# Kernel optimization log

Measured on AMD Instinct MI355X. Metric: run time of the kernel, lower is better.

The kernel has to match this reference:

```python
import jax, jax.numpy as jnp
import numpy as np

B, D = 8192, 1024

def setup_inputs() -> dict:
    key = jax.random.key(0)
    ks = jax.random.split(key, 5)
    scale = 1.0 / np.sqrt(D)
    return {
        "x": jax.random.normal(ks[0], (B, D), dtype=jnp.float32),
        "h": jax.random.normal(ks[1], (B, D), dtype=jnp.float32),
        "c": jax.random.normal(ks[2], (B, D), dtype=jnp.float32),
        # gate order: [input, forget, output, candidate]
        "Wx": jax.random.normal(ks[3], (4, D, D), dtype=jnp.float32) * scale,
        "Wh": jax.random.normal(ks[4], (4, D, D), dtype=jnp.float32) * scale,
    }

def reference(x, h, c, Wx, Wh):
    # two batched GEMMs covering all 8 projections: [B,D] x [4,D,D] -> [4,B,D]
    gx = jnp.einsum('bd,gdk->gbk', x, Wx)
    gh = jnp.einsum('bd,gdk->gbk', h, Wh)
    g = gx + gh
    i = jax.nn.sigmoid(g[0])
    f = jax.nn.sigmoid(g[1])
    o = jax.nn.sigmoid(g[2])
    u = jnp.tanh(g[3])
    c_t = i * u + f * c
    h_t = o * jnp.tanh(c_t)
    return (h_t, c_t)
```

## Files before the change

kernel.cpp:

```cpp
#include <hip/hip_runtime.h>
#include <hip/hip_bf16.h>
#include <cstdint>


#define LDS_TOTAL 131072

typedef __attribute__((ext_vector_type(8))) short bf16x8;
typedef __attribute__((ext_vector_type(4))) float f32x4;
typedef __attribute__((ext_vector_type(4))) unsigned int u32x4;

static __device__ __forceinline__ unsigned short f2bf(float f) {
  union { float f; unsigned int u; } v; v.f = f;
  unsigned int u = v.u;
  unsigned int r = (u + 0x7FFFu + ((u >> 16) & 1u)) >> 16;
  return (unsigned short)r;
}

static __device__ __forceinline__ void load16(const void* gp, void* lp) {
  __builtin_amdgcn_global_load_lds(
      (const __attribute__((address_space(1))) void*)gp,
      (__attribute__((address_space(3))) void*)lp, 16, 0, 0);
}

static __device__ __forceinline__ float sigmoid_f(float x) {
  return 1.0f / (1.0f + __expf(-x));
}
static __device__ __forceinline__ float tanh_f(float x) {
  float e = __expf(-2.0f * fabsf(x));
  float r = (1.0f - e) / (1.0f + e);
  return copysignf(r, x);
}

__global__ __launch_bounds__(256) void pack_a_kernel(
    const float* __restrict__ x, const float* __restrict__ h,
    unsigned short* __restrict__ Apack) {
  int t = blockIdx.x * 256 + threadIdx.x;
  size_t base = (size_t)t * 8;
  int b = (int)(base >> 11);
  int k = (int)(base & 2047);
  const float* src = (k < 1024) ? (x + (size_t)b * 1024 + k)
                                : (h + (size_t)b * 1024 + (k - 1024));
  float4 v0 = ((const float4*)src)[0];
  float4 v1 = ((const float4*)src)[1];
  union { unsigned short s[8]; u32x4 v; } o;
  o.s[0] = f2bf(v0.x); o.s[1] = f2bf(v0.y); o.s[2] = f2bf(v0.z); o.s[3] = f2bf(v0.w);
  o.s[4] = f2bf(v1.x); o.s[5] = f2bf(v1.y); o.s[6] = f2bf(v1.z); o.s[7] = f2bf(v1.w);
  *(u32x4*)(Apack + base) = o.v;
}

__global__ __launch_bounds__(256) void prep_w_kernel(
    const float* __restrict__ Wx, const float* __restrict__ Wh,
    unsigned short* __restrict__ Wt) {
  __shared__ float tile[32][33];
  int bid = blockIdx.x;
  int g = bid >> 11;
  int rem = bid & 2047;
  int kt = rem >> 5;
  int nt = rem & 31;
  int k0 = kt * 32, n0 = nt * 32;
  int tx = threadIdx.x & 31, ty = threadIdx.x >> 5;
  const float* Wsrc;
  int ks;
  if (k0 < 1024) { Wsrc = Wx + (size_t)g * 1048576; ks = k0; }
  else           { Wsrc = Wh + (size_t)g * 1048576; ks = k0 - 1024; }
  #pragma unroll
  for (int s = 0; s < 4; ++s) {
    int r = ty + s * 8;
    tile[r][tx] = Wsrc[(size_t)(ks + r) * 1024 + n0 + tx];
  }
  __syncthreads();
  #pragma unroll
  for (int s = 0; s < 4; ++s) {
    int r = ty + s * 8;
    Wt[(size_t)((g << 10) + n0 + r) * 2048 + k0 + tx] = f2bf(tile[tx][r]);
  }
}

__global__ __launch_bounds__(512, 2) void lstm_gemm_kernel(
    const unsigned short* __restrict__ Apack,
    const unsigned short* __restrict__ Wt,
    const float* __restrict__ cprev,
    float* __restrict__ out) {
  extern __shared__ char lds[];
  const int tid = threadIdx.x;
  const int l = tid & 63;
  const int w = tid >> 6;
  const int wr = w >> 2;
  const int wc = w & 3;
  const int bid0 = blockIdx.x;
  const int bid = (bid0 & 7) * 64 + (bid0 >> 3);
  const int mt = bid >> 4;
  const int nt = bid & 15;
  const int m0 = mt << 8;
  const int n0 = nt << 6;

  char* const buf0 = lds;
  char* const buf1 = lds + 65536;

  f32x4 acc[8][4];
  #pragma unroll
  for (int mf = 0; mf < 8; ++mf)
    #pragma unroll
    for (int g = 0; g < 4; ++g) acc[mf][g] = (f32x4)0.0f;

  bf16x8 aR[4][2];
  bf16x8 bR[4][2];

  const int lr = l & 15;
  const int kgrp = (l >> 4) << 4;
  const int sx = (lr & 7) << 4;
  const int kx0 = kgrp ^ sx;
  const int kx1 = (64 + kgrp) ^ sx;
  const int aoff = (wr * 128 + lr) * 128;
  const int boff = 32768 + (wc * 16 + lr) * 128;

  const int arl = tid >> 3;
  const int akb = ((tid << 4) & 127) ^ ((arl & 7) << 4);
  const unsigned short* const gAbase =
      Apack + (size_t)(m0 + arl) * 2048 + (akb >> 1);
  const int dAbase = (tid & ~63) << 4;
  const unsigned short* const gBbase =
      Wt + (size_t)(n0 + arl) * 2048 + (akb >> 1);
  const int dBbase = 32768 + ((tid & ~63) << 4);

  auto stageA = [&](char* bufb, int h, int kstep) {
    const unsigned short* g0 = gAbase + ((size_t)h * 262144 + (kstep << 6));
    #pragma unroll
    for (int j = 0; j < 2; ++j)
      load16(g0 + (size_t)j * 131072,
             bufb + dAbase + h * 16384 + j * 8192);
  };
  auto stageB = [&](char* bufb, int h, int kstep) {
    const unsigned short* g0 = gBbase + ((size_t)(2 * h) * 2097152 + (kstep << 6));
    #pragma unroll
    for (int j = 0; j < 2; ++j)
      load16(g0 + (size_t)j * 2097152,
             bufb + dBbase + h * 16384 + j * 8192);
  };

  auto readA = [&](const char* bufc, int mh) {
    #pragma unroll
    for (int i = 0; i < 4; ++i) {
      const char* p = bufc + aoff + (mh * 64 + i * 16) * 128;
      aR[i][0] = *(const bf16x8*)(p + kx0);
      aR[i][1] = *(const bf16x8*)(p + kx1);
    }
  };
  auto readB = [&](const char* bufc, int gh) {
    #pragma unroll
    for (int i = 0; i < 2; ++i) {
      const char* p = bufc + boff + (gh * 2 + i) * 8192;
      bR[gh * 2 + i][0] = *(const bf16x8*)(p + kx0);
      bR[gh * 2 + i][1] = *(const bf16x8*)(p + kx1);
    }
  };
  auto mfma16 = [&](int mh, int gh) {
    __builtin_amdgcn_s_setprio(1);
    #pragma unroll
    for (int kk = 0; kk < 2; ++kk)
      #pragma unroll
      for (int i = 0; i < 4; ++i)
        #pragma unroll
        for (int gg = 0; gg < 2; ++gg)
          acc[mh * 4 + i][gh * 2 + gg] = __builtin_amdgcn_mfma_f32_16x16x32_bf16(
              aR[i][kk], bR[gh * 2 + gg][kk], acc[mh * 4 + i][gh * 2 + gg], 0, 0, 0);
    __builtin_amdgcn_s_setprio(0);
  };

  stageA(buf0, 0, 0); stageA(buf0, 1, 0);
  stageB(buf0, 0, 0); stageB(buf0, 1, 0);
  stageB(buf1, 0, 1); stageB(buf1, 1, 1);
  stageA(buf1, 0, 1);
  asm volatile("s_waitcnt vmcnt(6)" ::: "memory");
  __builtin_amdgcn_s_barrier();

  auto kstep = [&](int t, char* bufc, char* bufn) {
    readA(bufc, 0);
    readB(bufc, 0);
    if (t + 1 < 32) stageA(bufn, 1, t + 1);
    asm volatile("s_waitcnt lgkmcnt(8)" ::: "memory");
    __builtin_amdgcn_s_barrier();
    asm volatile("s_waitcnt lgkmcnt(0)" ::: "memory");
    mfma16(0, 0);
    __builtin_amdgcn_s_barrier();
    readB(bufc, 1);
    if (t + 2 < 32) stageB(bufc, 0, t + 2);
    __builtin_amdgcn_s_barrier();
    asm volatile("s_waitcnt lgkmcnt(0)" ::: "memory");
    mfma16(0, 1);
    __builtin_amdgcn_s_barrier();
    readA(bufc, 1);
    if (t + 2 < 32) stageB(bufc, 1, t + 2);
    __builtin_amdgcn_s_barrier();
    asm volatile("s_waitcnt lgkmcnt(0)" ::: "memory");
    mfma16(1, 1);
    __builtin_amdgcn_s_barrier();
    if (t + 2 < 32) stageA(bufc, 0, t + 2);
    if (t < 30) asm volatile("s_waitcnt vmcnt(6)" ::: "memory");
    else        asm volatile("s_waitcnt vmcnt(0)" ::: "memory");
    __builtin_amdgcn_s_barrier();
    mfma16(1, 0);
    __builtin_amdgcn_s_barrier();
  };

  #pragma unroll 1
  for (int tt = 0; tt < 16; ++tt) {
    kstep(2 * tt,     buf0, buf1);
    kstep(2 * tt + 1, buf1, buf0);
  }

  const int q = (l >> 4) << 2;
  const int col = n0 + wc * 16 + lr;
  #pragma unroll
  for (int mf = 0; mf < 8; ++mf) {
    #pragma unroll
    for (int j = 0; j < 4; ++j) {
      int row = m0 + wr * 128 + mf * 16 + q + j;
      float gi = acc[mf][0][j];
      float gf = acc[mf][1][j];
      float go = acc[mf][2][j];
      float gu = acc[mf][3][j];
      float i_ = sigmoid_f(gi);
      float f_ = sigmoid_f(gf);
      float o_ = sigmoid_f(go);
      float u_ = tanh_f(gu);
      size_t idx = (size_t)row * 1024 + col;
      float ct = i_ * u_ + f_ * cprev[idx];
      float ht = o_ * tanh_f(ct);
      out[idx] = ht;
      out[8388608 + idx] = ct;
    }
  }
}

extern "C" void kernel_launch(void* const* d_in, const int* in_sizes, int n_in,
                              void* d_out, int out_size, void* d_ws, size_t ws_size,
                              hipStream_t stream) {
  const float* x  = (const float*)d_in[0];
  const float* h  = (const float*)d_in[1];
  const float* c  = (const float*)d_in[2];
  const float* Wx = (const float*)d_in[3];
  const float* Wh = (const float*)d_in[4];
  float* out = (float*)d_out;

  unsigned short* Apack = (unsigned short*)d_ws;
  unsigned short* Wt = (unsigned short*)((char*)d_ws + 33554432);

  hipFuncSetAttribute((const void*)lstm_gemm_kernel,
                      hipFuncAttributeMaxDynamicSharedMemorySize, LDS_TOTAL);

  pack_a_kernel<<<8192, 256, 0, stream>>>(x, h, Apack);
  prep_w_kernel<<<8192, 256, 0, stream>>>(Wx, Wh, Wt);
  lstm_gemm_kernel<<<dim3(512), dim3(512), LDS_TOTAL, stream>>>(Apack, Wt, c, out);
}
```

Baseline: 158.7 us.

## Shrink GEMM block tile to 128x32 with 256 threads and 2048 blocks

Halves the workgroup tile in both M and N (256x64x4 gates to 128x32x4 gates), uses 4 waves per block instead of 8, and launches 2048 blocks with 64KB of LDS instead of 512 blocks with 128KB. The k-step pipeline is restructured into two MFMA phases with new staging offsets. The aim is more blocks resident per CU and better load balance across CUs. The cost is lower arithmetic intensity per block, so each block reloads more A and W data from global memory for the same work.

After: 185.0 us. 16.6% more time.

```diff
diff --git a/kernel.cpp b/kernel.cpp
--- a/kernel.cpp
+++ b/kernel.cpp
@@ -3,7 +3,7 @@
 #include <cstdint>
 
 
-#define LDS_TOTAL 131072
+#define LDS_TOTAL 65536
 
 typedef __attribute__((ext_vector_type(8))) short bf16x8;
 typedef __attribute__((ext_vector_type(4))) float f32x4;
@@ -76,7 +76,7 @@
   }
 }
 
-__global__ __launch_bounds__(512, 2) void lstm_gemm_kernel(
+__global__ __launch_bounds__(256, 2) void lstm_gemm_kernel(
     const unsigned short* __restrict__ Apack,
     const unsigned short* __restrict__ Wt,
     const float* __restrict__ cprev,
@@ -85,21 +85,21 @@
   const int tid = threadIdx.x;
   const int l = tid & 63;
   const int w = tid >> 6;
-  const int wr = w >> 2;
-  const int wc = w & 3;
+  const int wr = w >> 1;
+  const int wc = w & 1;
   const int bid0 = blockIdx.x;
-  const int bid = (bid0 & 7) * 64 + (bid0 >> 3);
-  const int mt = bid >> 4;
-  const int nt = bid & 15;
-  const int m0 = mt << 8;
-  const int n0 = nt << 6;
+  const int bid = (bid0 & 7) * 256 + (bid0 >> 3);
+  const int mt = bid >> 5;
+  const int nt = bid & 31;
+  const int m0 = mt << 7;
+  const int n0 = nt << 5;
 
   char* const buf0 = lds;
-  char* const buf1 = lds + 65536;
-
-  f32x4 acc[8][4];
-  #pragma unroll
-  for (int mf = 0; mf < 8; ++mf)
+  char* const buf1 = lds + 32768;
+
+  f32x4 acc[4][4];
+  #pragma unroll
+  for (int mf = 0; mf < 4; ++mf)
     #pragma unroll
     for (int g = 0; g < 4; ++g) acc[mf][g] = (f32x4)0.0f;
 
@@ -111,37 +111,39 @@
   const int sx = (lr & 7) << 4;
   const int kx0 = kgrp ^ sx;
   const int kx1 = (64 + kgrp) ^ sx;
-  const int aoff = (wr * 128 + lr) * 128;
-  const int boff = 32768 + (wc * 16 + lr) * 128;
+  const int aoff = (wr * 64 + lr) * 128;
+  const int boff = 16384 + (wc * 16 + lr) * 128;
 
   const int arl = tid >> 3;
   const int akb = ((tid << 4) & 127) ^ ((arl & 7) << 4);
   const unsigned short* const gAbase =
       Apack + (size_t)(m0 + arl) * 2048 + (akb >> 1);
-  const int dAbase = (tid & ~63) << 4;
   const unsigned short* const gBbase =
       Wt + (size_t)(n0 + arl) * 2048 + (akb >> 1);
-  const int dBbase = 32768 + ((tid & ~63) << 4);
-
-  auto stageA = [&](char* bufb, int h, int kstep) {
-    const unsigned short* g0 = gAbase + ((size_t)h * 262144 + (kstep << 6));
-    #pragma unroll
-    for (int j = 0; j < 2; ++j)
-      load16(g0 + (size_t)j * 131072,
-             bufb + dAbase + h * 16384 + j * 8192);
-  };
-  auto stageB = [&](char* bufb, int h, int kstep) {
-    const unsigned short* g0 = gBbase + ((size_t)(2 * h) * 2097152 + (kstep << 6));
-    #pragma unroll
-    for (int j = 0; j < 2; ++j)
-      load16(g0 + (size_t)j * 2097152,
-             bufb + dBbase + h * 16384 + j * 8192);
-  };
-
-  auto readA = [&](const char* bufc, int mh) {
+  const int dbase = (tid & ~63) << 4;
+
+  auto stageA = [&](char* bufb, int t) {
+    const unsigned short* g0 = gAbase + (t << 6);
+    load16(g0,          bufb + dbase);
+    load16(g0 +  65536, bufb + dbase + 4096);
+    load16(g0 + 131072, bufb + dbase + 8192);
+    load16(g0 + 196608, bufb + dbase + 12288);
+  };
+  auto stageB0 = [&](char* bufb, int t) {
+    const unsigned short* g0 = gBbase + (t << 6);
+    load16(g0,           bufb + 16384 + dbase);
+    load16(g0 + 2097152, bufb + 20480 + dbase);
+  };
+  auto stageB1 = [&](char* bufb, int t) {
+    const unsigned short* g0 = gBbase + (size_t)2 * 2097152 + (t << 6);
+    load16(g0,           bufb + 24576 + dbase);
+    load16(g0 + 2097152, bufb + 28672 + dbase);
+  };
+
+  auto readA = [&](const char* bufc) {
     #pragma unroll
     for (int i = 0; i < 4; ++i) {
-      const char* p = bufc + aoff + (mh * 64 + i * 16) * 128;
+      const char* p = bufc + aoff + i * 2048;
       aR[i][0] = *(const bf16x8*)(p + kx0);
       aR[i][1] = *(const bf16x8*)(p + kx1);
     }
@@ -149,12 +151,12 @@
   auto readB = [&](const char* bufc, int gh) {
     #pragma unroll
     for (int i = 0; i < 2; ++i) {
-      const char* p = bufc + boff + (gh * 2 + i) * 8192;
+      const char* p = bufc + boff + (gh * 2 + i) * 4096;
       bR[gh * 2 + i][0] = *(const bf16x8*)(p + kx0);
       bR[gh * 2 + i][1] = *(const bf16x8*)(p + kx1);
     }
   };
-  auto mfma16 = [&](int mh, int gh) {
+  auto mfma16 = [&](int gh) {
     __builtin_amdgcn_s_setprio(1);
     #pragma unroll
     for (int kk = 0; kk < 2; ++kk)
@@ -162,44 +164,32 @@
       for (int i = 0; i < 4; ++i)
         #pragma unroll
         for (int gg = 0; gg < 2; ++gg)
-          acc[mh * 4 + i][gh * 2 + gg] = __builtin_amdgcn_mfma_f32_16x16x32_bf16(
-              aR[i][kk], bR[gh * 2 + gg][kk], acc[mh * 4 + i][gh * 2 + gg], 0, 0, 0);
+          acc[i][gh * 2 + gg] = __builtin_amdgcn_mfma_f32_16x16x32_bf16(
+              aR[i][kk], bR[gh * 2 + gg][kk], acc[i][gh * 2 + gg], 0, 0, 0);
     __builtin_amdgcn_s_setprio(0);
   };
 
-  stageA(buf0, 0, 0); stageA(buf0, 1, 0);
-  stageB(buf0, 0, 0); stageB(buf0, 1, 0);
-  stageB(buf1, 0, 1); stageB(buf1, 1, 1);
-  stageA(buf1, 0, 1);
+  stageA(buf0, 0); stageB0(buf0, 0); stageB1(buf0, 0);
+  stageA(buf1, 1); stageB0(buf1, 1);
   asm volatile("s_waitcnt vmcnt(6)" ::: "memory");
   __builtin_amdgcn_s_barrier();
 
   auto kstep = [&](int t, char* bufc, char* bufn) {
-    readA(bufc, 0);
+    readA(bufc);
     readB(bufc, 0);
-    if (t + 1 < 32) stageA(bufn, 1, t + 1);
+    if (t + 1 < 32) stageB1(bufn, t + 1);
     asm volatile("s_waitcnt lgkmcnt(8)" ::: "memory");
     __builtin_amdgcn_s_barrier();
     asm volatile("s_waitcnt lgkmcnt(0)" ::: "memory");
-    mfma16(0, 0);
+    mfma16(0);
     __builtin_amdgcn_s_barrier();
     readB(bufc, 1);
-    if (t + 2 < 32) stageB(bufc, 0, t + 2);
+    if (t + 2 < 32) { stageA(bufc, t + 2); stageB0(bufc, t + 2); }
     __builtin_amdgcn_s_barrier();
     asm volatile("s_waitcnt lgkmcnt(0)" ::: "memory");
-    mfma16(0, 1);
-    __builtin_amdgcn_s_barrier();
-    readA(bufc, 1);
-    if (t + 2 < 32) stageB(bufc, 1, t + 2);
-    __builtin_amdgcn_s_barrier();
-    asm volatile("s_waitcnt lgkmcnt(0)" ::: "memory");
-    mfma16(1, 1);
-    __builtin_amdgcn_s_barrier();
-    if (t + 2 < 32) stageA(bufc, 0, t + 2);
+    mfma16(1);
     if (t < 30) asm volatile("s_waitcnt vmcnt(6)" ::: "memory");
     else        asm volatile("s_waitcnt vmcnt(0)" ::: "memory");
-    __builtin_amdgcn_s_barrier();
-    mfma16(1, 0);
     __builtin_amdgcn_s_barrier();
   };
 
@@ -212,10 +202,10 @@
   const int q = (l >> 4) << 2;
   const int col = n0 + wc * 16 + lr;
   #pragma unroll
-  for (int mf = 0; mf < 8; ++mf) {
+  for (int mf = 0; mf < 4; ++mf) {
     #pragma unroll
     for (int j = 0; j < 4; ++j) {
-      int row = m0 + wr * 128 + mf * 16 + q + j;
+      int row = m0 + wr * 64 + mf * 16 + q + j;
       float gi = acc[mf][0][j];
       float gf = acc[mf][1][j];
       float go = acc[mf][2][j];
@@ -246,10 +236,7 @@
   unsigned short* Apack = (unsigned short*)d_ws;
   unsigned short* Wt = (unsigned short*)((char*)d_ws + 33554432);
 
-  hipFuncSetAttribute((const void*)lstm_gemm_kernel,
-                      hipFuncAttributeMaxDynamicSharedMemorySize, LDS_TOTAL);
-
   pack_a_kernel<<<8192, 256, 0, stream>>>(x, h, Apack);
   prep_w_kernel<<<8192, 256, 0, stream>>>(Wx, Wh, Wt);
-  lstm_gemm_kernel<<<dim3(512), dim3(512), LDS_TOTAL, stream>>>(Apack, Wt, c, out);
-}
+  lstm_gemm_kernel<<<dim3(2048), dim3(256), LDS_TOTAL, stream>>>(Apack, Wt, c, out);
+}
```
